# Optimization experiments

Measured on AMD Instinct MI355X. Metric: run time of the kernel, lower is better.

## Reference

```python
import jax, jax.numpy as jnp
import numpy as np

# Tsit5 Butcher tableau (Tsitouras 2011), b7 = 0 for the accepted solution.
_C = (0.161, 0.327, 0.9, 0.9800255409045097, 1.0)
_A = (
    (0.161,),
    (-0.008480655492356989, 0.335480655492357),
    (2.8971530571054935, -6.359448489975075, 4.3622954328695815),
    (5.325864828439257, -11.748883564062828, 7.4955393428898365, -0.09249506636175525),
    (5.86145544294642, -12.92096931784711, 8.159367898576159, -0.071584973281401, -0.028269050394068383),
)
_B = (0.09646076681806523, 0.01, 0.4798896504144996, 1.379008574103742, -3.290069515436081, 2.324710524099774)

K_STEPS, BATCH, N_STATE, N_INPUT, HIDDEN = 512, 64, 128, 32, 256


def setup_inputs() -> dict:
    key = jax.random.key(0)
    k1, k2, k3, k4 = jax.random.split(key, 4)
    ts = jnp.linspace(0.0, 1.0, K_STEPS, dtype=jnp.float32)
    y0 = jax.random.normal(k1, (BATCH, N_STATE), dtype=jnp.float32)
    us = jax.random.normal(k2, (BATCH, K_STEPS, N_INPUT), dtype=jnp.float32)
    fan_in = 1 + N_STATE + N_INPUT  # t, y, u
    W1 = jax.random.normal(k3, (HIDDEN, fan_in), dtype=jnp.float32) / np.sqrt(fan_in)
    b1 = jnp.zeros((HIDDEN,), dtype=jnp.float32)
    W2 = jax.random.normal(k4, (N_STATE, HIDDEN), dtype=jnp.float32) / np.sqrt(HIDDEN)
    b2 = jnp.zeros((N_STATE,), dtype=jnp.float32)
    return {"ts": ts, "y0": y0, "us": us, "W1": W1, "b1": b1, "W2": W2, "b2": b2}


def _solve(ts, y0_i, us_i, W1, b1, W2, b2):
    """Integrate one trajectory with fixed-step Tsit5 on the save grid."""
    dt_grid = jnp.diff(ts)                              # (k-1,)
    # backward-Hermite derivative estimates for the input signal u(t)
    d = jnp.diff(us_i, axis=0) / dt_grid[:, None]       # (k-1, m)
    d = jnp.concatenate([d[:1], d], axis=0)             # (k, m)

    def func(t, y, u):
        z = jnp.concatenate([t[None], y, u])
        return W2 @ jnp.tanh(W1 @ z + b1) + b2

    def u_at(i, theta):
        # cubic Hermite interpolation of u on interval [ts[i], ts[i+1]]
        h = dt_grid[i]
        u0, u1, d0, d1 = us_i[i], us_i[i + 1], d[i], d[i + 1]
        t2 = theta * theta
        t3 = t2 * theta
        return ((2 * t3 - 3 * t2 + 1) * u0 + (t3 - 2 * t2 + theta) * h * d0
                + (-2 * t3 + 3 * t2) * u1 + (t3 - t2) * h * d1)

    def step(y, i):
        t0, h = ts[i], dt_grid[i]
        ks = []
        k = func(t0, y, u_at(i, jnp.float32(0.0)))
        ks.append(k)
        for c, arow in zip(_C, _A):
            ytmp = y + h * sum(a * kj for a, kj in zip(arow, ks))
            ks.append(func(t0 + c * h, ytmp, u_at(i, jnp.float32(c))))
        y_new = y + h * sum(b * kj for b, kj in zip(_B, ks))
        return y_new, y_new

    _, ys = jax.lax.scan(step, y0_i, jnp.arange(ts.shape[0] - 1))
    return jnp.concatenate([y0_i[None], ys], axis=0)    # (k, n)


def reference(ts, y0, us, W1, b1, W2, b2):
    return jax.vmap(_solve, in_axes=(None, 0, 0, None, None, None, None))(
        ts, y0, us, W1, b1, W2, b2
    )
```

## Files before the change

kernel.cpp:

```cpp
#include <hip/hip_runtime.h>

namespace {

typedef _Float16 h2 __attribute__((ext_vector_type(2)));
typedef _Float16 f16x8 __attribute__((ext_vector_type(8)));
typedef float    f32x4 __attribute__((ext_vector_type(4)));

constexpr int KSTEPS = 512;
constexpr int NSTATE = 128;
constexpr int NINPUT = 32;
constexpr int HID    = 256;
constexpr int FANIN  = 161;
constexpr int BATCH  = 64;
constexpr int CHUNK  = 64;
constexpr int NCH    = 8;

constexpr size_t WS_M  = 0;
constexpr size_t WS_C  = WS_M + (size_t)HID * HID * 2;
constexpr size_t WS_US = WS_C + HID * 4;
constexpr size_t WS_HB = WS_US + (size_t)BATCH * KSTEPS * NINPUT * 2;
constexpr size_t WS_T  = WS_HB + (size_t)BATCH * KSTEPS * HID * 2;

__device__ __forceinline__ float fdot2(h2 a, h2 b, float c) {
#if __has_builtin(__builtin_amdgcn_fdot2)
  return __builtin_amdgcn_fdot2(a, b, c, false);
#else
  return c + (float)a[0] * (float)b[0] + (float)a[1] * (float)b[1];
#endif
}

__device__ __forceinline__ float fast_tanh(float x) {
  float e2 = __builtin_amdgcn_exp2f(x * 2.8853900817779268f);
  float r  = __builtin_amdgcn_rcpf(e2 + 1.0f);
  return __builtin_fmaf(-2.0f, r, 1.0f);
}

#define BAR() __asm__ volatile("s_waitcnt lgkmcnt(0)\n\ts_barrier" ::: "memory")

union F4 { float4 f; h2 h[4]; };

__global__ __launch_bounds__(256)
void k1_compose(const float* __restrict__ W1, const float* __restrict__ W2,
                const float* __restrict__ b2, _Float16* __restrict__ wsM,
                float* __restrict__ wsC) {
  const int j  = blockIdx.x;
  const int hc = threadIdx.x;
  const float* w1row = W1 + (size_t)j * FANIN + 1;
  float acc = 0.0f;
  for (int o = 0; o < NSTATE; ++o)
    acc = __builtin_fmaf(w1row[o], W2[(size_t)o * HID + hc], acc);
  wsM[(size_t)j * HID + hc] = (_Float16)acc;
  if (hc == 0) {
    float ca = 0.0f;
    for (int o = 0; o < NSTATE; ++o) ca = __builtin_fmaf(w1row[o], b2[o], ca);
    wsC[j] = ca;
  }
}

__global__ __launch_bounds__(256)
void k1b_transcode(const float* __restrict__ us, _Float16* __restrict__ us16) {
  const size_t idx = ((size_t)blockIdx.x * 256 + threadIdx.x) * 4;
  const float4 v = *(const float4*)(us + idx);
  us16[idx + 0] = (_Float16)v.x;
  us16[idx + 1] = (_Float16)v.y;
  us16[idx + 2] = (_Float16)v.z;
  us16[idx + 3] = (_Float16)v.w;
}

__global__ __launch_bounds__(512)
__attribute__((amdgpu_waves_per_eu(2, 2)))
void k2_main(const float* __restrict__ ts,
             const float* __restrict__ y0,
             const float* __restrict__ W1,
             const float* __restrict__ b1,
             char* __restrict__ ws)
{
  const int lt = threadIdx.x;
  const int w  = lt >> 6;
  const int ln = lt & 63;
  const int c  = ln & 15;
  const int q  = (ln >> 4) & 3;
  const int klo = q * 8;
  const int j  = 32 * w + 16 * (c & 1) + 4 * q + ((c >> 1) & 3);
  const bool wrl = (c < 8);
  const int b  = blockIdx.x;

  const _Float16* wsM  = (const _Float16*)(ws + WS_M);
  const float*    wsC  = (const float*)(ws + WS_C);
  const _Float16* us16 = (const _Float16*)(ws + WS_US) + (size_t)b * KSTEPS * NINPUT;
  _Float16*       wsHB = (_Float16*)(ws + WS_HB) + (size_t)b * KSTEPS * HID;
  float*          wsT  = (float*)(ws + WS_T) + (size_t)b * NCH * HID;

  __shared__ __align__(16) _Float16 hbuf[2][HID];
  __shared__ __align__(16) float y0s[NSTATE];
  __shared__ __align__(16) float tss[KSTEPS];
  __shared__ __align__(16) _Float16 usl[KSTEPS * NINPUT];

  {
    const F4* src = (const F4*)us16;
    F4* dst = (F4*)usl;
    #pragma unroll
    for (int it = 0; it < 4; ++it) dst[lt + 512 * it] = src[lt + 512 * it];
    tss[lt] = ts[lt];
  }

  f16x8 af[2][8];
  #pragma unroll
  for (int t = 0; t < 2; ++t) {
    const int row = 32 * w + 16 * t + (ln & 15);
    #pragma unroll
    for (int kk = 0; kk < 8; ++kk)
      af[t][kk] = *(const f16x8*)(wsM + (size_t)row * HID + kk * 32 + klo);
  }

  const float* w1row = W1 + (size_t)j * FANIN;
  const float  w1t   = w1row[0];
  h2 w1u[16];
  #pragma unroll
  for (int i = 0; i < 16; ++i)
    w1u[i] = h2{(_Float16)w1row[129 + 2 * i], (_Float16)w1row[130 + 2 * i]};
  const float cR = wsC[j];

  if (lt < NSTATE) y0s[lt] = y0[(size_t)b * NSTATE + lt];
  __syncthreads();
  float P = b1[j];
  {
    const float* wy = w1row + 1;
    #pragma unroll 8
    for (int o = 0; o < NSTATE; ++o) P = __builtin_fmaf(wy[o], y0s[o], P);
  }

  constexpr double CcD[5] = {0.161, 0.327, 0.9, 0.9800255409045097, 1.0};
  constexpr float Af[5][5] = {
    {0.161f, 0.f, 0.f, 0.f, 0.f},
    {-0.008480655492356989f, 0.335480655492357f, 0.f, 0.f, 0.f},
    {2.8971530571054935f, -6.359448489975075f, 4.3622954328695815f, 0.f, 0.f},
    {5.325864828439257f, -11.748883564062828f, 7.4955393428898365f, -0.09249506636175525f, 0.f},
    {5.86145544294642f, -12.92096931784711f, 8.159367898576159f, -0.071584973281401f,
     -0.028269050394068383f}};
  constexpr float Bf[6] = {0.09646076681806523f, 0.01f, 0.4798896504144996f,
                           1.379008574103742f, -3.290069515436081f, 2.324710524099774f};

  float Ua, Ub = 0.0f, Uaprev = 0.0f, D = 0.0f;
  {
    const F4* up = (const F4*)(usl);
    F4 u0 = up[0], u1 = up[1], u2 = up[2], u3 = up[3];
    float s = 0.0f;
    #pragma unroll
    for (int i = 0; i < 4; ++i) {
      s = fdot2(w1u[i],      u0.h[i], s);
      s = fdot2(w1u[4 + i],  u1.h[i], s);
      s = fdot2(w1u[8 + i],  u2.h[i], s);
      s = fdot2(w1u[12 + i], u3.h[i], s);
    }
    Ua = s;
  }

  float tcur = ts[0], tn1 = ts[1];
  float dtp = 1.0f;
  float h0v = fast_tanh(P + Ua + w1t * tcur);
  if (wrl) hbuf[0][j] = (_Float16)h0v;
  float hB = Bf[0] * h0v;
  float Sacc = 0.0f;
  float aR[6];

  for (int i = 0; i < KSTEPS - 1; ++i) {
    const float dt = tn1 - tcur;
    const int   i2 = (i + 2 < KSTEPS) ? (i + 2) : (KSTEPS - 1);
    const float tn2 = tss[i2];
    F4 ur0, ur1, ur2, ur3;
    {
      const F4* up = (const F4*)(&usl[(i + 1) * NINPUT]);
      ur0 = up[0]; ur1 = up[1]; ur2 = up[2]; ur3 = up[3];
    }

    if (i > 0 && (i & (CHUNK - 1)) == 0 && wrl)
      wsT[(size_t)(i >> 6) * HID + j] = Sacc;

    #pragma unroll
    for (int e = 0; e < 6; ++e) {
      BAR();

      if (e == 5 && wrl) {
        wsHB[(size_t)i * HID + j] = (_Float16)hB;
      }
      if (e == 0) {
        float s = 0.0f;
        #pragma unroll
        for (int qq = 0; qq < 4; ++qq) {
          s = fdot2(w1u[qq],      ur0.h[qq], s);
          s = fdot2(w1u[4 + qq],  ur1.h[qq], s);
          s = fdot2(w1u[8 + qq],  ur2.h[qq], s);
          s = fdot2(w1u[12 + qq], ur3.h[qq], s);
        }
        Ub = s;
        D = (i == 0) ? (Ub - Ua)
                     : (Ua - Uaprev) * (dt * __builtin_amdgcn_rcpf(dtp));
      }

      const _Float16* hb = hbuf[e & 1];
      f32x4 ac0 = {0.f, 0.f, 0.f, 0.f};
      f32x4 ac1 = {0.f, 0.f, 0.f, 0.f};
      #pragma unroll
      for (int kk = 0; kk < 8; ++kk) {
        const f16x8 bf = *(const f16x8*)(hb + kk * 32 + klo);
        ac0 = __builtin_amdgcn_mfma_f32_16x16x32_f16(af[0][kk], bf, ac0, 0, 0, 0);
        ac1 = __builtin_amdgcn_mfma_f32_16x16x32_f16(af[1][kk], bf, ac1, 0, 0, 0);
      }
      float ae;
      {
        const bool tsel = (c & 1) != 0;
        float v0 = tsel ? ac1[0] : ac0[0];
        float v1 = tsel ? ac1[1] : ac0[1];
        float v2 = tsel ? ac1[2] : ac0[2];
        float v3 = tsel ? ac1[3] : ac0[3];
        const bool r0 = (c & 2) != 0;
        const bool r1 = (c & 4) != 0;
        ae = r1 ? (r0 ? v3 : v2) : (r0 ? v1 : v0);
      }
      ae += cR;
      aR[e] = ae;

      if (e < 5) {
        float acm = 0.0f;
        #pragma unroll
        for (int mm = 0; mm <= e; ++mm) acm = __builtin_fmaf(Af[e][mm], aR[mm], acm);
        const double th = CcD[e];
        const float cu0 = (float)(th * th * th - 2.0 * th * th + 1.0);
        const float cu1 = (float)(2.0 * th * th - th * th * th);
        const float cd0 = (float)(th * th * th - 2.0 * th * th + th);
        const float ut  = cu0 * Ua + cu1 * Ub + cd0 * D;
        const float te  = __builtin_fmaf((float)th, dt, tcur);
        float pre = __builtin_fmaf(dt, acm, P) + ut;
        pre = __builtin_fmaf(w1t, te, pre);
        const float hv = fast_tanh(pre);
        if (wrl) hbuf[(e + 1) & 1][j] = (_Float16)hv;
        hB = __builtin_fmaf(Bf[e + 1], hv, hB);
      } else {
        float acm = 0.0f;
        #pragma unroll
        for (int mm = 0; mm < 6; ++mm) acm = __builtin_fmaf(Bf[mm], aR[mm], acm);
        P = __builtin_fmaf(dt, acm, P);
        Sacc = __builtin_fmaf(dt, hB, Sacc);
        float pre = P + Ub;
        pre = __builtin_fmaf(w1t, tn1, pre);
        const float hv = fast_tanh(pre);
        if (wrl) hbuf[0][j] = (_Float16)hv;
        hB = Bf[0] * hv;
      }
    }

    Uaprev = Ua; Ua = Ub;
    dtp = dt; tcur = tn1; tn1 = tn2;
  }
}

__global__ __launch_bounds__(256, 1)
void k4_out(const float* __restrict__ ts,
            const float* __restrict__ y0,
            const float* __restrict__ W2,
            const char* __restrict__ ws,
            float* __restrict__ out)
{
  const int blk = blockIdx.x;
  const int b = blk >> 3;
  const int c = blk & 7;
  const int lt = threadIdx.x;
  const int o    = lt >> 1;
  const int half = lt & 1;

  const _Float16* wsHB = (const _Float16*)(ws + WS_HB) + (size_t)b * KSTEPS * HID;
  const float*    wsT  = (const float*)(ws + WS_T) + (size_t)b * NCH * HID;
  float* outb = out + (size_t)b * KSTEPS * NSTATE;

  __shared__ __align__(16) _Float16 Sb[HID];

  h2 w2r[64];
  {
    const float* row = W2 + (size_t)o * HID + 128 * half;
    #pragma unroll
    for (int i = 0; i < 64; ++i)
      w2r[i] = h2{(_Float16)row[2 * i], (_Float16)row[2 * i + 1]};
  }
  const float y0o = y0[(size_t)b * NSTATE + o];
  if (c == 0 && lt < NSTATE) outb[lt] = y0[(size_t)b * NSTATE + lt];

  float S = (c > 0) ? wsT[(size_t)c * HID + lt] : 0.0f;
  const int i0 = c * CHUNK;
  const int n  = (KSTEPS - 1 - i0 < CHUNK) ? (KSTEPS - 1 - i0) : CHUNK;

  float tc = ts[i0], tn = ts[i0 + 1];
  float hcur = (float)wsHB[(size_t)i0 * HID + lt];
  for (int l = 0; l < n; ++l) {
    const int i = i0 + l;
    const int inx = (i + 1 < KSTEPS - 1) ? (i + 1) : (KSTEPS - 2);
    const float hnext = (float)wsHB[(size_t)inx * HID + lt];
    const float tnn = ts[(i + 2 < KSTEPS) ? (i + 2) : (KSTEPS - 1)];

    const float dt = tn - tc;
    S = __builtin_fmaf(dt, hcur, S);
    Sb[lt] = (_Float16)S;
    __syncthreads();

    const F4* sp = (const F4*)(&Sb[128 * half]);
    float v0 = 0.0f, v1 = 0.0f;
    #pragma unroll
    for (int q = 0; q < 16; ++q) {
      F4 sc = sp[q];
      v0 = fdot2(w2r[4 * q + 0], sc.h[0], v0);
      v1 = fdot2(w2r[4 * q + 1], sc.h[1], v1);
      v0 = fdot2(w2r[4 * q + 2], sc.h[2], v0);
      v1 = fdot2(w2r[4 * q + 3], sc.h[3], v1);
    }
    float v = v0 + v1;
    v += __shfl_xor(v, 1);
    if (half == 0) outb[(size_t)(i + 1) * NSTATE + o] = y0o + v;
    __syncthreads();

    hcur = hnext; tc = tn; tn = tnn;
  }
}

}

extern "C" void kernel_launch(void* const* d_in, const int* in_sizes, int n_in,
                              void* d_out, int out_size, void* d_ws, size_t ws_size,
                              hipStream_t stream) {
  const float* ts = (const float*)d_in[0];
  const float* y0 = (const float*)d_in[1];
  const float* us = (const float*)d_in[2];
  const float* W1 = (const float*)d_in[3];
  const float* b1 = (const float*)d_in[4];
  const float* W2 = (const float*)d_in[5];
  const float* b2 = (const float*)d_in[6];
  float* out = (float*)d_out;
  char* ws = (char*)d_ws;

  _Float16* wsM  = (_Float16*)(ws + WS_M);
  float*    wsC  = (float*)(ws + WS_C);
  _Float16* us16 = (_Float16*)(ws + WS_US);

  hipLaunchKernelGGL(k1_compose, dim3(HID), dim3(HID), 0, stream, W1, W2, b2, wsM, wsC);
  hipLaunchKernelGGL(k1b_transcode, dim3(BATCH * KSTEPS * NINPUT / 1024), dim3(256),
                     0, stream, us, us16);
  hipLaunchKernelGGL(k2_main, dim3(BATCH), dim3(512), 0, stream, ts, y0, W1, b1, ws);
  hipLaunchKernelGGL(k4_out, dim3(BATCH * NCH), dim3(256), 0, stream, ts, y0, W2,
                     (const char*)ws, out);
}
```

Baseline: 1.591 ms.

## Pack two trajectories per block using idle MFMA columns

The main integration kernel now processes two trajectories per workgroup and launches half as many blocks. Lanes whose MFMA output columns were previously redundant (c >= 8) now carry the second trajectory's hidden-state vector, and the hidden buffers are duplicated per trajectory and padded. The B-operand loads are also hoisted ahead of the MFMA chain. This uses otherwise wasted matrix throughput and frees CUs. Because the kernel is a serial, latency-bound recurrence, per-step latency may not shrink, and the doubled LDS footprint could cost occupancy.

```diff
diff --git a/kernel.cpp b/kernel.cpp
--- a/kernel.cpp
+++ b/kernel.cpp
@@ -75,32 +75,38 @@
              const float* __restrict__ b1,
              char* __restrict__ ws)
 {
-  const int lt = threadIdx.x;
-  const int w  = lt >> 6;
-  const int ln = lt & 63;
-  const int c  = ln & 15;
-  const int q  = (ln >> 4) & 3;
+  const int lt  = threadIdx.x;
+  const int w   = lt >> 6;
+  const int ln  = lt & 63;
+  const int c   = ln & 15;
+  const int q   = ln >> 4;
   const int klo = q * 8;
-  const int j  = 32 * w + 16 * (c & 1) + 4 * q + ((c >> 1) & 3);
-  const bool wrl = (c < 8);
-  const int b  = blockIdx.x;
+  const int traj = c >> 3;
+  const int j   = 32 * w + 16 * (c & 1) + 4 * q + ((c >> 1) & 3);
+  const int blk = blockIdx.x;
+  const int b   = 2 * blk + traj;
 
   const _Float16* wsM  = (const _Float16*)(ws + WS_M);
   const float*    wsC  = (const float*)(ws + WS_C);
-  const _Float16* us16 = (const _Float16*)(ws + WS_US) + (size_t)b * KSTEPS * NINPUT;
+  const _Float16* usbase = (const _Float16*)(ws + WS_US) + (size_t)(2 * blk) * KSTEPS * NINPUT;
   _Float16*       wsHB = (_Float16*)(ws + WS_HB) + (size_t)b * KSTEPS * HID;
   float*          wsT  = (float*)(ws + WS_T) + (size_t)b * NCH * HID;
 
-  __shared__ __align__(16) _Float16 hbuf[2][HID];
-  __shared__ __align__(16) float y0s[NSTATE];
+  __shared__ __align__(16) _Float16 hbuf[2][2][272];
+  __shared__ __align__(16) float y0s[2][NSTATE];
   __shared__ __align__(16) float tss[KSTEPS];
-  __shared__ __align__(16) _Float16 usl[KSTEPS * NINPUT];
+  __shared__ __align__(16) _Float16 usl[2][KSTEPS * NINPUT];
 
   {
-    const F4* src = (const F4*)us16;
-    F4* dst = (F4*)usl;
-    #pragma unroll
-    for (int it = 0; it < 4; ++it) dst[lt + 512 * it] = src[lt + 512 * it];
+    const F4* s0 = (const F4*)(usbase);
+    const F4* s1 = (const F4*)(usbase + (size_t)KSTEPS * NINPUT);
+    F4* d0 = (F4*)usl[0];
+    F4* d1 = (F4*)usl[1];
+    #pragma unroll
+    for (int it = 0; it < 4; ++it) {
+      d0[lt + 512 * it] = s0[lt + 512 * it];
+      d1[lt + 512 * it] = s1[lt + 512 * it];
+    }
     tss[lt] = ts[lt];
   }
 
@@ -121,13 +127,14 @@
     w1u[i] = h2{(_Float16)w1row[129 + 2 * i], (_Float16)w1row[130 + 2 * i]};
   const float cR = wsC[j];
 
-  if (lt < NSTATE) y0s[lt] = y0[(size_t)b * NSTATE + lt];
+  if (lt < 2 * NSTATE)
+    y0s[lt >> 7][lt & 127] = y0[(size_t)(2 * blk + (lt >> 7)) * NSTATE + (lt & 127)];
   __syncthreads();
   float P = b1[j];
   {
     const float* wy = w1row + 1;
     #pragma unroll 8
-    for (int o = 0; o < NSTATE; ++o) P = __builtin_fmaf(wy[o], y0s[o], P);
+    for (int o = 0; o < NSTATE; ++o) P = __builtin_fmaf(wy[o], y0s[traj][o], P);
   }
 
   constexpr double CcD[5] = {0.161, 0.327, 0.9, 0.9800255409045097, 1.0};
@@ -143,7 +150,7 @@
 
   float Ua, Ub = 0.0f, Uaprev = 0.0f, D = 0.0f;
   {
-    const F4* up = (const F4*)(usl);
+    const F4* up = (const F4*)(usl[traj]);
     F4 u0 = up[0], u1 = up[1], u2 = up[2], u3 = up[3];
     float s = 0.0f;
     #pragma unroll
@@ -159,7 +166,7 @@
   float tcur = ts[0], tn1 = ts[1];
   float dtp = 1.0f;
   float h0v = fast_tanh(P + Ua + w1t * tcur);
-  if (wrl) hbuf[0][j] = (_Float16)h0v;
+  hbuf[traj][0][j] = (_Float16)h0v;
   float hB = Bf[0] * h0v;
   float Sacc = 0.0f;
   float aR[6];
@@ -170,18 +177,24 @@
     const float tn2 = tss[i2];
     F4 ur0, ur1, ur2, ur3;
     {
-      const F4* up = (const F4*)(&usl[(i + 1) * NINPUT]);
+      const F4* up = (const F4*)(&usl[traj][(i + 1) * NINPUT]);
       ur0 = up[0]; ur1 = up[1]; ur2 = up[2]; ur3 = up[3];
     }
 
-    if (i > 0 && (i & (CHUNK - 1)) == 0 && wrl)
+    if (i > 0 && (i & (CHUNK - 1)) == 0)
       wsT[(size_t)(i >> 6) * HID + j] = Sacc;
 
     #pragma unroll
     for (int e = 0; e < 6; ++e) {
       BAR();
 
-      if (e == 5 && wrl) {
+      const _Float16* hb = hbuf[traj][e & 1];
+      f16x8 bf[8];
+      #pragma unroll
+      for (int kk = 0; kk < 8; ++kk)
+        bf[kk] = *(const f16x8*)(hb + kk * 32 + klo);
+
+      if (e == 5) {
         wsHB[(size_t)i * HID + j] = (_Float16)hB;
       }
       if (e == 0) {
@@ -198,14 +211,12 @@
                      : (Ua - Uaprev) * (dt * __builtin_amdgcn_rcpf(dtp));
       }
 
-      const _Float16* hb = hbuf[e & 1];
       f32x4 ac0 = {0.f, 0.f, 0.f, 0.f};
       f32x4 ac1 = {0.f, 0.f, 0.f, 0.f};
       #pragma unroll
       for (int kk = 0; kk < 8; ++kk) {
-        const f16x8 bf = *(const f16x8*)(hb + kk * 32 + klo);
-        ac0 = __builtin_amdgcn_mfma_f32_16x16x32_f16(af[0][kk], bf, ac0, 0, 0, 0);
-        ac1 = __builtin_amdgcn_mfma_f32_16x16x32_f16(af[1][kk], bf, ac1, 0, 0, 0);
+        ac0 = __builtin_amdgcn_mfma_f32_16x16x32_f16(af[0][kk], bf[kk], ac0, 0, 0, 0);
+        ac1 = __builtin_amdgcn_mfma_f32_16x16x32_f16(af[1][kk], bf[kk], ac1, 0, 0, 0);
       }
       float ae;
       {
@@ -234,7 +245,7 @@
         float pre = __builtin_fmaf(dt, acm, P) + ut;
         pre = __builtin_fmaf(w1t, te, pre);
         const float hv = fast_tanh(pre);
-        if (wrl) hbuf[(e + 1) & 1][j] = (_Float16)hv;
+        hbuf[traj][(e + 1) & 1][j] = (_Float16)hv;
         hB = __builtin_fmaf(Bf[e + 1], hv, hB);
       } else {
         float acm = 0.0f;
@@ -245,7 +256,7 @@
         float pre = P + Ub;
         pre = __builtin_fmaf(w1t, tn1, pre);
         const float hv = fast_tanh(pre);
-        if (wrl) hbuf[0][j] = (_Float16)hv;
+        hbuf[traj][0][j] = (_Float16)hv;
         hB = Bf[0] * hv;
       }
     }
@@ -343,7 +354,7 @@
   hipLaunchKernelGGL(k1_compose, dim3(HID), dim3(HID), 0, stream, W1, W2, b2, wsM, wsC);
   hipLaunchKernelGGL(k1b_transcode, dim3(BATCH * KSTEPS * NINPUT / 1024), dim3(256),
                      0, stream, us, us16);
-  hipLaunchKernelGGL(k2_main, dim3(BATCH), dim3(512), 0, stream, ts, y0, W1, b1, ws);
+  hipLaunchKernelGGL(k2_main, dim3(BATCH / 2), dim3(512), 0, stream, ts, y0, W1, b1, ws);
   hipLaunchKernelGGL(k4_out, dim3(BATCH * NCH), dim3(256), 0, stream, ts, y0, W2,
                      (const char*)ws, out);
 }
```

Measured after the change: 1.536 ms (median of 2 runs). 3.5% less time.
